# Kernel tuning notes

Hardware: AMD Instinct MI355X
Metric: run time of the kernel (lower is better)

Reference implementation:

```python
import jax, jax.numpy as jnp
import numpy as np

N_NODES = 50000
N_EDGES = 800000
IN_CH = 256
HID = 512
NUM_LAYERS = 3
EPS = 1e-12  # F.normalize eps


def setup_inputs() -> dict:
    key = jax.random.key(0)
    ks = jax.random.split(key, 2 + 3 * NUM_LAYERS)
    x = jax.random.normal(ks[0], (N_NODES, IN_CH), dtype=jnp.float32)
    edge_index = jax.random.randint(ks[1], (2, N_EDGES), 0, N_NODES, dtype=jnp.int64)
    inp = {"x": x, "edge_index": edge_index}
    dims = [(IN_CH, HID)] + [(HID, HID)] * (NUM_LAYERS - 1)
    for i, (din, dout) in enumerate(dims):
        s = 1.0 / np.sqrt(din)
        inp[f"Wl{i}"] = jax.random.normal(ks[2 + 3 * i], (din, dout), dtype=jnp.float32) * s
        inp[f"bl{i}"] = jnp.zeros((dout,), dtype=jnp.float32)
        inp[f"Wr{i}"] = jax.random.normal(ks[3 + 3 * i], (din, dout), dtype=jnp.float32) * s
    return inp


def _sage_conv(x, src, dst, Wl, bl, Wr):
    # aggr='add': out[dst] += x[src], then lin_l(agg) + lin_r(x), L2 normalize rows
    agg = jax.ops.segment_sum(x[src], dst, num_segments=x.shape[0])  # [N, din]
    out = agg @ Wl + bl + x @ Wr  # [N, dout]
    norm = jnp.maximum(jnp.linalg.norm(out, axis=-1, keepdims=True), EPS)
    return out / norm


def reference(x, edge_index, Wl0, bl0, Wr0, Wl1, bl1, Wr1, Wl2, bl2, Wr2):
    src, dst = edge_index[0], edge_index[1]
    feat = x
    params = [(Wl0, bl0, Wr0), (Wl1, bl1, Wr1), (Wl2, bl2, Wr2)]
    for Wl, bl, Wr in params:
        aggre = _sage_conv(feat, src, dst, Wl, bl, Wr)
        # Dropout(p=0.15) is identity in eval mode
        feat = jax.nn.elu(aggre)
    return feat
```

## Files before the change

kernel.cpp:

```cpp
#include <hip/hip_runtime.h>
#include <math.h>

#define N_NODES 50000
#define M_PAD   50048
#define N_EDGES 800000
#define HID 512

typedef short bf16x8 __attribute__((ext_vector_type(8)));
typedef float f32x4  __attribute__((ext_vector_type(4)));
typedef unsigned short u16x4 __attribute__((ext_vector_type(4)));
typedef unsigned short u16x8 __attribute__((ext_vector_type(8)));

__device__ inline float b2f(unsigned short u) {
    union { unsigned int i; float f; } v; v.i = ((unsigned int)u) << 16; return v.f;
}
__device__ inline unsigned short f2b(float f) {
    union { float f; unsigned int i; } v; v.f = f;
    unsigned int r = v.i + 0x7FFFu + ((v.i >> 16) & 1u);
    return (unsigned short)(r >> 16);
}


__global__ void zero_kernel(int* __restrict__ p, int n) {
    int i = blockIdx.x * blockDim.x + threadIdx.x;
    if (i < n) p[i] = 0;
}

__global__ void detect_kernel(const int* __restrict__ e, int* __restrict__ flag) {
    if (blockIdx.x == 0 && threadIdx.x == 0) {
        int is64 = 1;
        for (int i = 0; i < 16; ++i)
            if (e[2 * i + 1] != 0) is64 = 0;
        *flag = is64;
    }
}

__global__ void hist_kernel(const void* __restrict__ eidx, const int* __restrict__ flag,
                            int* __restrict__ counts) {
    int e = blockIdx.x * blockDim.x + threadIdx.x;
    if (e >= N_EDGES) return;
    int is64 = *flag;
    int d;
    if (is64) d = (int)((const long long*)eidx)[N_EDGES + e];
    else      d = ((const int*)eidx)[N_EDGES + e];
    atomicAdd(&counts[d], 1);
}

__global__ __launch_bounds__(1024) void scan_kernel(const int* __restrict__ counts,
                                                    int* __restrict__ offsets) {
    __shared__ int sums[1024];
    int t = threadIdx.x;
    const int CH = (N_NODES + 1023) / 1024;
    int lo = t * CH;
    int hi = min(lo + CH, N_NODES);
    int s = 0;
    for (int i = lo; i < hi; ++i) s += counts[i];
    sums[t] = s;
    __syncthreads();
    for (int off = 1; off < 1024; off <<= 1) {
        int v = 0;
        if (t >= off) v = sums[t - off];
        __syncthreads();
        sums[t] += v;
        __syncthreads();
    }
    int excl = (t == 0) ? 0 : sums[t - 1];
    for (int i = lo; i < hi; ++i) { offsets[i] = excl; excl += counts[i]; }
    if (t == 1023) offsets[N_NODES] = excl;
}

__global__ void fill_kernel(const void* __restrict__ eidx, const int* __restrict__ flag,
                            const int* __restrict__ offsets, int* __restrict__ cursor,
                            int* __restrict__ edge_src) {
    int e = blockIdx.x * blockDim.x + threadIdx.x;
    if (e >= N_EDGES) return;
    int is64 = *flag;
    int s, d;
    if (is64) {
        const long long* p = (const long long*)eidx;
        s = (int)p[e];
        d = (int)p[N_EDGES + e];
    } else {
        const int* p = (const int*)eidx;
        s = p[e];
        d = p[N_EDGES + e];
    }
    int pos = atomicAdd(&cursor[d], 1);
    edge_src[offsets[d] + pos] = s;
}


__global__ __launch_bounds__(256) void xconv_kernel(const float* __restrict__ x,
                                                    unsigned short* __restrict__ cat1) {
    int id = blockIdx.x * 256 + threadIdx.x;
    if (id >= M_PAD * 64) return;
    int row = id >> 6;
    int c = (id & 63) * 4;
    float4 v = make_float4(0.f, 0.f, 0.f, 0.f);
    if (row < N_NODES) v = *(const float4*)(x + (size_t)row * 256 + c);
    ushort4 h;
    h.x = f2b(v.x); h.y = f2b(v.y); h.z = f2b(v.z); h.w = f2b(v.w);
    *(ushort4*)(cat1 + (size_t)row * 512 + 256 + c) = h;
}

__global__ __launch_bounds__(128) void wconv_kernel(const float* __restrict__ W,
                                                    unsigned short* __restrict__ T,
                                                    int K, int ktot, int off) {
    int n = blockIdx.x;
    for (int k = threadIdx.x; k < K; k += 128)
        T[(size_t)n * ktot + off + k] = f2b(W[(size_t)k * HID + n]);
}


template <int EPL>
__global__ __launch_bounds__(256) void aggregate_kernel(const unsigned short* __restrict__ Fh,
                                                        const int* __restrict__ off,
                                                        const int* __restrict__ esrc,
                                                        unsigned short* __restrict__ Ah) {
    const int W = EPL * 64;
    const int STRIDE = 2 * W;
    const int wid = threadIdx.x >> 6;
    const int lane = threadIdx.x & 63;
    const int node = blockIdx.x * 4 + wid;
    if (node >= N_NODES) return;
    const int beg = off[node], end = off[node + 1];
    const int deg = end - beg;

    float a0[EPL], a1[EPL], a2[EPL], a3[EPL];
#pragma unroll
    for (int j = 0; j < EPL; ++j) { a0[j] = 0.f; a1[j] = 0.f; a2[j] = 0.f; a3[j] = 0.f; }

    const int lb = lane * EPL;
    int idxv = 0;

#define ACC(ARR, S)                                                         \
    {                                                                       \
        const unsigned short* r_ = Fh + (size_t)(S) * STRIDE + lb;          \
        if constexpr (EPL == 8) {                                           \
            u16x8 v_ = *(const u16x8*)r_;                                   \
            _Pragma("unroll")                                               \
            for (int j_ = 0; j_ < 8; ++j_) ARR[j_] += b2f(v_[j_]);          \
        } else {                                                            \
            u16x4 v_ = *(const u16x4*)r_;                                   \
            _Pragma("unroll")                                               \
            for (int j_ = 0; j_ < 4; ++j_) ARR[j_] += b2f(v_[j_]);          \
        }                                                                   \
    }

    for (int i = 0; i < deg; i += 4) {
        const int b = i & 63;
        if (b == 0) idxv = (beg + i + lane < end) ? esrc[beg + i + lane] : 0;
        const int s0 = __shfl(idxv, b);
        const int s1 = __shfl(idxv, b + 1);
        const int s2 = __shfl(idxv, b + 2);
        const int s3 = __shfl(idxv, b + 3);
        ACC(a0, s0);
        if (i + 1 < deg) ACC(a1, s1);
        if (i + 2 < deg) ACC(a2, s2);
        if (i + 3 < deg) ACC(a3, s3);
    }
#undef ACC

    unsigned short* op = Ah + (size_t)node * STRIDE + lb;
    if constexpr (EPL == 8) {
        u16x8 h;
#pragma unroll
        for (int j = 0; j < 8; ++j) h[j] = f2b(a0[j] + a1[j] + a2[j] + a3[j]);
        __builtin_nontemporal_store(h, (u16x8*)op);
    } else {
        u16x4 h;
#pragma unroll
        for (int j = 0; j < 4; ++j) h[j] = f2b(a0[j] + a1[j] + a2[j] + a3[j]);
        __builtin_nontemporal_store(h, (u16x4*)op);
    }
}


template <int FINAL>
__global__ __launch_bounds__(256, 4) void gemm_mfma_kernel(
    const unsigned short* __restrict__ A, const unsigned short* __restrict__ B,
    const float* __restrict__ bias, float* __restrict__ outF,
    unsigned short* __restrict__ pre, int K) {
    __shared__ unsigned short S[2 * 8192];
    const int bm = blockIdx.y * 128;
    const int bn = blockIdx.x * 128;
    const int tid = threadIdx.x;
    const int l = tid & 63;
    const int w = tid >> 6;
    const int wr = (w >> 1) * 64;
    const int wc = (w & 1) * 64;
    const int arow = l >> 2;
    const int acol = (l & 3) * 8;

    const unsigned short* gA = A + (size_t)(bm + arow) * K + acol;
    const unsigned short* gB = B + (size_t)(bn + arow) * K + acol;

    f32x4 acc[4][4];
#pragma unroll
    for (int m = 0; m < 4; ++m)
#pragma unroll
        for (int n = 0; n < 4; ++n) acc[m][n] = (f32x4){0.f, 0.f, 0.f, 0.f};

    const int aoff = (wr + (l & 15)) * 32 + (l >> 4) * 8;
    const int woff = (wc + (l & 15)) * 32 + (l >> 4) * 8;
    const int ktiles = K >> 5;

    auto STAGE = [&](int buf, int kt) {
        unsigned short* lb = &S[buf * 8192];
#pragma unroll
        for (int i = 0; i < 2; ++i) {
            const int c = w * 2 + i;
            __builtin_amdgcn_global_load_lds(
                (const __attribute__((address_space(1))) void*)(gA + (size_t)(c * 16) * K + kt * 32),
                (__attribute__((address_space(3))) void*)(lb + c * 512), 16, 0, 0);
            __builtin_amdgcn_global_load_lds(
                (const __attribute__((address_space(1))) void*)(gB + (size_t)(c * 16) * K + kt * 32),
                (__attribute__((address_space(3))) void*)(lb + 4096 + c * 512), 16, 0, 0);
        }
    };

    auto COMPUTE = [&](int sb) {
        bf16x8 af[4], wf[4];
#pragma unroll
        for (int m = 0; m < 4; ++m)
            af[m] = *(const bf16x8*)&S[sb + aoff + m * 512];
#pragma unroll
        for (int n = 0; n < 4; ++n)
            wf[n] = *(const bf16x8*)&S[sb + 4096 + woff + n * 512];
#pragma unroll
        for (int m = 0; m < 4; ++m)
#pragma unroll
            for (int n = 0; n < 4; ++n)
                acc[m][n] = __builtin_amdgcn_mfma_f32_16x16x32_bf16(af[m], wf[n], acc[m][n], 0, 0, 0);
    };

    STAGE(0, 0);
    for (int kt = 0; kt < ktiles - 1; ++kt) {
        STAGE((kt + 1) & 1, kt + 1);
        asm volatile("s_waitcnt vmcnt(4)" ::: "memory");
        __builtin_amdgcn_s_barrier();
        __builtin_amdgcn_sched_barrier(0);
        COMPUTE((kt & 1) * 8192);
        __builtin_amdgcn_s_barrier();
    }
    asm volatile("s_waitcnt vmcnt(0)" ::: "memory");
    __builtin_amdgcn_s_barrier();
    __builtin_amdgcn_sched_barrier(0);
    COMPUTE(((ktiles - 1) & 1) * 8192);

    const int r0 = bm + wr + (l >> 4) * 4;
    const int c0 = bn + wc + (l & 15);
#pragma unroll
    for (int n = 0; n < 4; ++n) {
        const float bv = bias[c0 + n * 16];
#pragma unroll
        for (int m = 0; m < 4; ++m) {
#pragma unroll
            for (int j = 0; j < 4; ++j) {
                int gr = r0 + m * 16 + j;
                if (gr < N_NODES) {
                    float val = acc[m][n][j] + bv;
                    if constexpr (FINAL)
                        __builtin_nontemporal_store(val, &outF[(size_t)gr * HID + c0 + n * 16]);
                    else
                        __builtin_nontemporal_store(f2b(val), &pre[(size_t)gr * HID + c0 + n * 16]);
                }
            }
        }
    }
}


template <int FINAL>
__global__ __launch_bounds__(256) void norm_elu_kernel(const void* __restrict__ inp,
                                                       float* __restrict__ outF,
                                                       unsigned short* __restrict__ Fh) {
    const int wid = threadIdx.x >> 6;
    const int lane = threadIdx.x & 63;
    const int row = blockIdx.x * 4 + wid;
    if (row >= N_NODES) return;
    float r[8];
    if constexpr (FINAL) {
        const float* p = (const float*)inp + (size_t)row * HID + lane * 8;
        float4 v0 = *(const float4*)p;
        float4 v1 = *(const float4*)(p + 4);
        r[0] = v0.x; r[1] = v0.y; r[2] = v0.z; r[3] = v0.w;
        r[4] = v1.x; r[5] = v1.y; r[6] = v1.z; r[7] = v1.w;
    } else {
        const unsigned short* p = (const unsigned short*)inp + (size_t)row * HID + lane * 8;
        u16x8 v = *(const u16x8*)p;
#pragma unroll
        for (int j = 0; j < 8; ++j) r[j] = b2f(v[j]);
    }
    float ss = 0.f;
#pragma unroll
    for (int j = 0; j < 8; ++j) ss += r[j] * r[j];
#pragma unroll
    for (int o = 32; o > 0; o >>= 1) ss += __shfl_xor(ss, o);
    float inv = 1.f / fmaxf(sqrtf(ss), 1e-12f);
#pragma unroll
    for (int j = 0; j < 8; ++j) {
        r[j] *= inv;
        r[j] = r[j] > 0.f ? r[j] : expm1f(r[j]);
    }
    if constexpr (FINAL) {
        float* q = outF + (size_t)row * HID + lane * 8;
        *(float4*)q = make_float4(r[0], r[1], r[2], r[3]);
        *(float4*)(q + 4) = make_float4(r[4], r[5], r[6], r[7]);
    } else {
        unsigned short* q = Fh + (size_t)row * 1024 + lane * 8;
        u16x8 h;
#pragma unroll
        for (int j = 0; j < 8; ++j) h[j] = f2b(r[j]);
        *(u16x8*)q = h;
    }
}


extern "C" void kernel_launch(void* const* d_in, const int* in_sizes, int n_in,
                              void* d_out, int out_size, void* d_ws, size_t ws_size,
                              hipStream_t stream) {
    const float* x    = (const float*)d_in[0];
    const void*  eidx = d_in[1];
    const float* Wl0 = (const float*)d_in[2];
    const float* bl0 = (const float*)d_in[3];
    const float* Wr0 = (const float*)d_in[4];
    const float* Wl1 = (const float*)d_in[5];
    const float* bl1 = (const float*)d_in[6];
    const float* Wr1 = (const float*)d_in[7];
    const float* Wl2 = (const float*)d_in[8];
    const float* bl2 = (const float*)d_in[9];
    const float* Wr2 = (const float*)d_in[10];
    float* outF = (float*)d_out;
    unsigned short* preB = (unsigned short*)d_out;

    char* ws = (char*)d_ws;
    size_t o = 0;
    auto alloc = [&](size_t bytes) { void* p = ws + o; o += (bytes + 255) & ~(size_t)255; return p; };

    unsigned short* Cat1 = (unsigned short*)alloc((size_t)M_PAD * 512 * 2);
    unsigned short* Cat2 = (unsigned short*)alloc((size_t)M_PAD * 1024 * 2);

    unsigned short* Wcat0 = (unsigned short*)alloc(512 * 512 * 2);
    unsigned short* Wcat1 = (unsigned short*)alloc(512 * 1024 * 2);
    unsigned short* Wcat2 = (unsigned short*)alloc(512 * 1024 * 2);

    int* counts   = (int*)alloc((size_t)2 * N_NODES * 4);
    int* cursor   = counts + N_NODES;
    int* offsets  = (int*)alloc((size_t)(N_NODES + 1) * 4);
    int* edge_src = (int*)alloc((size_t)N_EDGES * 4);
    int* flag     = (int*)alloc(256);

    zero_kernel<<<(2 * N_NODES + 255) / 256, 256, 0, stream>>>(counts, 2 * N_NODES);
    detect_kernel<<<1, 64, 0, stream>>>((const int*)eidx, flag);
    hist_kernel<<<(N_EDGES + 255) / 256, 256, 0, stream>>>(eidx, flag, counts);
    scan_kernel<<<1, 1024, 0, stream>>>(counts, offsets);
    fill_kernel<<<(N_EDGES + 255) / 256, 256, 0, stream>>>(eidx, flag, offsets, cursor, edge_src);

    xconv_kernel<<<(M_PAD * 64 + 255) / 256, 256, 0, stream>>>(x, Cat1);
    wconv_kernel<<<512, 128, 0, stream>>>(Wl0, Wcat0, 256, 512, 0);
    wconv_kernel<<<512, 128, 0, stream>>>(Wr0, Wcat0, 256, 512, 256);
    wconv_kernel<<<512, 128, 0, stream>>>(Wl1, Wcat1, 512, 1024, 0);
    wconv_kernel<<<512, 128, 0, stream>>>(Wr1, Wcat1, 512, 1024, 512);
    wconv_kernel<<<512, 128, 0, stream>>>(Wl2, Wcat2, 512, 1024, 0);
    wconv_kernel<<<512, 128, 0, stream>>>(Wr2, Wcat2, 512, 1024, 512);

    dim3 ggrid(4, M_PAD / 128);
    const int ngrid = (N_NODES + 3) / 4;

    aggregate_kernel<4><<<ngrid, 256, 0, stream>>>(Cat1 + 256, offsets, edge_src, Cat1);
    gemm_mfma_kernel<0><<<ggrid, 256, 0, stream>>>(Cat1, Wcat0, bl0, nullptr, preB, 512);
    norm_elu_kernel<0><<<ngrid, 256, 0, stream>>>(preB, nullptr, Cat2 + 512);

    aggregate_kernel<8><<<ngrid, 256, 0, stream>>>(Cat2 + 512, offsets, edge_src, Cat2);
    gemm_mfma_kernel<0><<<ggrid, 256, 0, stream>>>(Cat2, Wcat1, bl1, nullptr, preB, 1024);
    norm_elu_kernel<0><<<ngrid, 256, 0, stream>>>(preB, nullptr, Cat2 + 512);

    aggregate_kernel<8><<<ngrid, 256, 0, stream>>>(Cat2 + 512, offsets, edge_src, Cat2);
    gemm_mfma_kernel<1><<<ggrid, 256, 0, stream>>>(Cat2, Wcat2, bl2, outF, nullptr, 1024);
    norm_elu_kernel<1><<<ngrid, 256, 0, stream>>>(outF, outF, nullptr);

    (void)in_sizes; (void)n_in; (void)out_size; (void)ws_size;
}
```

Before: 847.1 us.

## Batch aggregation loads eight-wide and widen GEMM tile to 128x256 with 512 threads

The aggregation loop now issues eight independent row loads per iteration before accumulating, with a scalar tail loop, to raise memory-level parallelism in the gather. The GEMM moves to 512-thread blocks computing 128x256 tiles, one load per thread per matrix slice, and a simpler __syncthreads double-buffer schedule in place of explicit waitcnt/barrier control. Output stores drop the nontemporal hint. The wider tile reuses each A tile across more columns, but the schedule change may expose more load latency and register pressure rises with 8 vector loads in flight.

```diff
diff --git a/kernel.cpp b/kernel.cpp
--- a/kernel.cpp
+++ b/kernel.cpp
@@ -117,83 +117,76 @@
                                                         const int* __restrict__ off,
                                                         const int* __restrict__ esrc,
                                                         unsigned short* __restrict__ Ah) {
-    const int W = EPL * 64;
-    const int STRIDE = 2 * W;
+    const int STRIDE = 2 * EPL * 64;
     const int wid = threadIdx.x >> 6;
     const int lane = threadIdx.x & 63;
     const int node = blockIdx.x * 4 + wid;
     if (node >= N_NODES) return;
     const int beg = off[node], end = off[node + 1];
     const int deg = end - beg;
-
-    float a0[EPL], a1[EPL], a2[EPL], a3[EPL];
-#pragma unroll
-    for (int j = 0; j < EPL; ++j) { a0[j] = 0.f; a1[j] = 0.f; a2[j] = 0.f; a3[j] = 0.f; }
-
     const int lb = lane * EPL;
+    using VecT = typename std::conditional<EPL == 8, u16x8, u16x4>::type;
+
+    float a0[EPL], a1[EPL];
+#pragma unroll
+    for (int j = 0; j < EPL; ++j) { a0[j] = 0.f; a1[j] = 0.f; }
+
     int idxv = 0;
-
-#define ACC(ARR, S)                                                         \
-    {                                                                       \
-        const unsigned short* r_ = Fh + (size_t)(S) * STRIDE + lb;          \
-        if constexpr (EPL == 8) {                                           \
-            u16x8 v_ = *(const u16x8*)r_;                                   \
-            _Pragma("unroll")                                               \
-            for (int j_ = 0; j_ < 8; ++j_) ARR[j_] += b2f(v_[j_]);          \
-        } else {                                                            \
-            u16x4 v_ = *(const u16x4*)r_;                                   \
-            _Pragma("unroll")                                               \
-            for (int j_ = 0; j_ < 4; ++j_) ARR[j_] += b2f(v_[j_]);          \
-        }                                                                   \
-    }
-
-    for (int i = 0; i < deg; i += 4) {
+    int i = 0;
+    for (; i + 8 <= deg; i += 8) {
         const int b = i & 63;
         if (b == 0) idxv = (beg + i + lane < end) ? esrc[beg + i + lane] : 0;
-        const int s0 = __shfl(idxv, b);
-        const int s1 = __shfl(idxv, b + 1);
-        const int s2 = __shfl(idxv, b + 2);
-        const int s3 = __shfl(idxv, b + 3);
-        ACC(a0, s0);
-        if (i + 1 < deg) ACC(a1, s1);
-        if (i + 2 < deg) ACC(a2, s2);
-        if (i + 3 < deg) ACC(a3, s3);
-    }
-#undef ACC
+        int s[8];
+#pragma unroll
+        for (int k = 0; k < 8; ++k) s[k] = __shfl(idxv, b + k);
+        VecT v[8];
+#pragma unroll
+        for (int k = 0; k < 8; ++k)
+            v[k] = *(const VecT*)(Fh + (size_t)s[k] * STRIDE + lb);
+#pragma unroll
+        for (int k = 0; k < 8; ++k) {
+#pragma unroll
+            for (int j = 0; j < EPL; ++j) {
+                if (k & 1) a1[j] += b2f(v[k][j]);
+                else       a0[j] += b2f(v[k][j]);
+            }
+        }
+    }
+    for (; i < deg; ++i) {
+        const int b = i & 63;
+        if (b == 0) idxv = (beg + i + lane < end) ? esrc[beg + i + lane] : 0;
+        const int s = __shfl(idxv, b);
+        VecT v = *(const VecT*)(Fh + (size_t)s * STRIDE + lb);
+#pragma unroll
+        for (int j = 0; j < EPL; ++j) a0[j] += b2f(v[j]);
+    }
 
     unsigned short* op = Ah + (size_t)node * STRIDE + lb;
-    if constexpr (EPL == 8) {
-        u16x8 h;
-#pragma unroll
-        for (int j = 0; j < 8; ++j) h[j] = f2b(a0[j] + a1[j] + a2[j] + a3[j]);
-        __builtin_nontemporal_store(h, (u16x8*)op);
-    } else {
-        u16x4 h;
-#pragma unroll
-        for (int j = 0; j < 4; ++j) h[j] = f2b(a0[j] + a1[j] + a2[j] + a3[j]);
-        __builtin_nontemporal_store(h, (u16x4*)op);
-    }
+    VecT h;
+#pragma unroll
+    for (int j = 0; j < EPL; ++j) h[j] = f2b(a0[j] + a1[j]);
+    __builtin_nontemporal_store(h, (VecT*)op);
 }
 
 
 template <int FINAL>
-__global__ __launch_bounds__(256, 4) void gemm_mfma_kernel(
+__global__ __launch_bounds__(512, 2) void gemm_mfma_kernel(
     const unsigned short* __restrict__ A, const unsigned short* __restrict__ B,
     const float* __restrict__ bias, float* __restrict__ outF,
     unsigned short* __restrict__ pre, int K) {
-    __shared__ unsigned short S[2 * 8192];
+    __shared__ unsigned short S[2 * 12288];
     const int bm = blockIdx.y * 128;
-    const int bn = blockIdx.x * 128;
+    const int bn = blockIdx.x * 256;
     const int tid = threadIdx.x;
     const int l = tid & 63;
     const int w = tid >> 6;
-    const int wr = (w >> 1) * 64;
-    const int wc = (w & 1) * 64;
-    const int arow = l >> 2;
-    const int acol = (l & 3) * 8;
-
-    const unsigned short* gA = A + (size_t)(bm + arow) * K + acol;
-    const unsigned short* gB = B + (size_t)(bn + arow) * K + acol;
+    const int wr = (w >> 2) * 64;
+    const int wc = (w & 3) * 64;
+
+    const int se = (tid >> 2) * 32 + (tid & 3) * 8;
+    const unsigned short* gA  = A + (size_t)(bm + (tid >> 2)) * K + (tid & 3) * 8;
+    const unsigned short* gB0 = B + (size_t)(bn + (tid >> 2)) * K + (tid & 3) * 8;
+    const unsigned short* gB1 = B + (size_t)(bn + 128 + (tid >> 2)) * K + (tid & 3) * 8;
 
     f32x4 acc[4][4];
 #pragma unroll
@@ -202,51 +195,43 @@
         for (int n = 0; n < 4; ++n) acc[m][n] = (f32x4){0.f, 0.f, 0.f, 0.f};
 
     const int aoff = (wr + (l & 15)) * 32 + (l >> 4) * 8;
-    const int woff = (wc + (l & 15)) * 32 + (l >> 4) * 8;
+    const int woff = 4096 + (wc + (l & 15)) * 32 + (l >> 4) * 8;
     const int ktiles = K >> 5;
 
     auto STAGE = [&](int buf, int kt) {
-        unsigned short* lb = &S[buf * 8192];
-#pragma unroll
-        for (int i = 0; i < 2; ++i) {
-            const int c = w * 2 + i;
-            __builtin_amdgcn_global_load_lds(
-                (const __attribute__((address_space(1))) void*)(gA + (size_t)(c * 16) * K + kt * 32),
-                (__attribute__((address_space(3))) void*)(lb + c * 512), 16, 0, 0);
-            __builtin_amdgcn_global_load_lds(
-                (const __attribute__((address_space(1))) void*)(gB + (size_t)(c * 16) * K + kt * 32),
-                (__attribute__((address_space(3))) void*)(lb + 4096 + c * 512), 16, 0, 0);
-        }
+        unsigned short* lb = &S[buf * 12288];
+        __builtin_amdgcn_global_load_lds(
+            (const __attribute__((address_space(1))) void*)(gA + kt * 32),
+            (__attribute__((address_space(3))) void*)(lb + se), 16, 0, 0);
+        __builtin_amdgcn_global_load_lds(
+            (const __attribute__((address_space(1))) void*)(gB0 + kt * 32),
+            (__attribute__((address_space(3))) void*)(lb + 4096 + se), 16, 0, 0);
+        __builtin_amdgcn_global_load_lds(
+            (const __attribute__((address_space(1))) void*)(gB1 + kt * 32),
+            (__attribute__((address_space(3))) void*)(lb + 8192 + se), 16, 0, 0);
     };
 
-    auto COMPUTE = [&](int sb) {
+    STAGE(0, 0);
+    __syncthreads();
+
+    for (int kt = 0; kt < ktiles; ++kt) {
+        if (kt + 1 < ktiles) STAGE((kt + 1) & 1, kt + 1);
+        const int sb = (kt & 1) * 12288;
+
         bf16x8 af[4], wf[4];
 #pragma unroll
         for (int m = 0; m < 4; ++m)
             af[m] = *(const bf16x8*)&S[sb + aoff + m * 512];
 #pragma unroll
         for (int n = 0; n < 4; ++n)
-            wf[n] = *(const bf16x8*)&S[sb + 4096 + woff + n * 512];
+            wf[n] = *(const bf16x8*)&S[sb + woff + n * 512];
 #pragma unroll
         for (int m = 0; m < 4; ++m)
 #pragma unroll
             for (int n = 0; n < 4; ++n)
                 acc[m][n] = __builtin_amdgcn_mfma_f32_16x16x32_bf16(af[m], wf[n], acc[m][n], 0, 0, 0);
-    };
-
-    STAGE(0, 0);
-    for (int kt = 0; kt < ktiles - 1; ++kt) {
-        STAGE((kt + 1) & 1, kt + 1);
-        asm volatile("s_waitcnt vmcnt(4)" ::: "memory");
-        __builtin_amdgcn_s_barrier();
-        __builtin_amdgcn_sched_barrier(0);
-        COMPUTE((kt & 1) * 8192);
-        __builtin_amdgcn_s_barrier();
-    }
-    asm volatile("s_waitcnt vmcnt(0)" ::: "memory");
-    __builtin_amdgcn_s_barrier();
-    __builtin_amdgcn_sched_barrier(0);
-    COMPUTE(((ktiles - 1) & 1) * 8192);
+        __syncthreads();
+    }
 
     const int r0 = bm + wr + (l >> 4) * 4;
     const int c0 = bn + wc + (l & 15);
@@ -261,9 +246,9 @@
                 if (gr < N_NODES) {
                     float val = acc[m][n][j] + bv;
                     if constexpr (FINAL)
-                        __builtin_nontemporal_store(val, &outF[(size_t)gr * HID + c0 + n * 16]);
+                        outF[(size_t)gr * HID + c0 + n * 16] = val;
                     else
-                        __builtin_nontemporal_store(f2b(val), &pre[(size_t)gr * HID + c0 + n * 16]);
+                        pre[(size_t)gr * HID + c0 + n * 16] = f2b(val);
                 }
             }
         }
@@ -365,19 +350,19 @@
     wconv_kernel<<<512, 128, 0, stream>>>(Wl2, Wcat2, 512, 1024, 0);
     wconv_kernel<<<512, 128, 0, stream>>>(Wr2, Wcat2, 512, 1024, 512);
 
-    dim3 ggrid(4, M_PAD / 128);
+    dim3 ggrid(2, M_PAD / 128);
     const int ngrid = (N_NODES + 3) / 4;
 
     aggregate_kernel<4><<<ngrid, 256, 0, stream>>>(Cat1 + 256, offsets, edge_src, Cat1);
-    gemm_mfma_kernel<0><<<ggrid, 256, 0, stream>>>(Cat1, Wcat0, bl0, nullptr, preB, 512);
+    gemm_mfma_kernel<0><<<ggrid, 512, 0, stream>>>(Cat1, Wcat0, bl0, nullptr, preB, 512);
     norm_elu_kernel<0><<<ngrid, 256, 0, stream>>>(preB, nullptr, Cat2 + 512);
 
     aggregate_kernel<8><<<ngrid, 256, 0, stream>>>(Cat2 + 512, offsets, edge_src, Cat2);
-    gemm_mfma_kernel<0><<<ggrid, 256, 0, stream>>>(Cat2, Wcat1, bl1, nullptr, preB, 1024);
+    gemm_mfma_kernel<0><<<ggrid, 512, 0, stream>>>(Cat2, Wcat1, bl1, nullptr, preB, 1024);
     norm_elu_kernel<0><<<ngrid, 256, 0, stream>>>(preB, nullptr, Cat2 + 512);
 
     aggregate_kernel<8><<<ngrid, 256, 0, stream>>>(Cat2 + 512, offsets, edge_src, Cat2);
-    gemm_mfma_kernel<1><<<ggrid, 256, 0, stream>>>(Cat2, Wcat2, bl2, outF, nullptr, 1024);
+    gemm_mfma_kernel<1><<<ggrid, 512, 0, stream>>>(Cat2, Wcat2, bl2, outF, nullptr, 1024);
     norm_elu_kernel<1><<<ngrid, 256, 0, stream>>>(outF, outF, nullptr);
 
     (void)in_sizes; (void)n_in; (void)out_size; (void)ws_size;
```

Result: faster. 784.8 us (-7.4%).
